# Optimization experiments

Measured on AMD Instinct MI355X. Metric: run time of the kernel, lower is better.

## Reference

```python
import jax, jax.numpy as jnp
import numpy as np

EPS = 1e-5  # nn.RMSNorm eps


def setup_inputs() -> dict:
    key = jax.random.key(0)
    ks = jax.random.split(key, 8)
    B, L, D, R = 4, 4096, 2048, 4
    return {
        "h": jax.random.normal(ks[0], (B, L, D), jnp.float32),
        "h_o": jax.random.normal(ks[1], (B, L, D), jnp.float32),
        "static_alpha": jax.random.normal(ks[2], (R, R + 1), jnp.float32),
        "static_beta": jax.random.normal(ks[3], (R,), jnp.float32),
        "dynamic_alpha_fn": jax.random.normal(ks[4], (D, R + 1), jnp.float32) * 0.02,
        "dynamic_alpha_scale": jax.random.uniform(ks[5], (1,), jnp.float32, 0.005, 0.02),
        "dynamic_beta_fn": jax.random.normal(ks[6], (D,), jnp.float32) * 0.02,
        "dynamic_beta_scale": jnp.array([0.01], jnp.float32),
        "rms_weight": jax.random.uniform(ks[7], (D,), jnp.float32, 0.5, 1.5),
    }


def reference(h, h_o, static_alpha, static_beta, dynamic_alpha_fn,
              dynamic_alpha_scale, dynamic_beta_fn, dynamic_beta_scale,
              rms_weight):
    # RMSNorm over last dim with learnable weight (dynamic branch only)
    h_norm = h * jax.lax.rsqrt(jnp.mean(h * h, axis=-1, keepdims=True) + EPS) * rms_weight

    # dynamic alpha: [B,L,rate+1] offset broadcast against static [rate,rate+1]
    alpha_offset = jnp.tanh(h_norm @ dynamic_alpha_fn) * dynamic_alpha_scale  # [B,L,R+1]
    alpha = alpha_offset[:, :, None, :] + static_alpha                        # [B,L,R,R+1]

    # dynamic beta: scalar offset per token broadcast against static [rate]
    beta_offset = jnp.tanh(h_norm @ dynamic_beta_fn) * dynamic_beta_scale     # [B,L] * [1]
    beta = beta_offset[..., None] + static_beta                               # [B,L,R]

    # connect_width: mix_h[b,l,c,d] = sum_r alpha[b,l,r,c] * h[b,l,d]
    mix_h = jnp.einsum('blrc,bld->blcd', alpha, h)                            # [B,L,R+1,D]

    # connect_depth: broadcast outer product beta x h_o plus old streams, sum over rate
    out = jnp.sum(beta[..., None] * h_o[:, :, None, :] + mix_h[:, :, 1:, :], axis=2)
    return out  # [B,L,D]
```

## Files before the change

### kernel.cpp

```cpp
#include <hip/hip_runtime.h>
#include <math.h>


constexpr int D    = 2048;
constexpr int RATE = 4;
constexpr float EPS = 1e-5f;
constexpr int TPB  = 8;
constexpr int NT   = 512;

__device__ __forceinline__ float fast_tanh(float x) {
    const float e = __expf(2.0f * x);
    return 1.0f - 2.0f / (e + 1.0f);
}

template<int CTRL>
__device__ __forceinline__ float dpp_add(float x) {
    int m = __builtin_amdgcn_update_dpp(0, __float_as_int(x), CTRL, 0xf, 0xf, true);
    return x + __int_as_float(m);
}

__device__ __forceinline__ float wave_sum_lane63(float x) {
    x = dpp_add<0x111>(x);
    x = dpp_add<0x112>(x);
    x = dpp_add<0x114>(x);
    x = dpp_add<0x118>(x);
    x = dpp_add<0x142>(x);
    x = dpp_add<0x143>(x);
    return x;
}

__device__ __forceinline__ void lds_barrier() {
    asm volatile("s_waitcnt lgkmcnt(0)" ::: "memory");
    __builtin_amdgcn_s_barrier();
    __builtin_amdgcn_sched_barrier(0);
}

__global__ __launch_bounds__(NT) void hyperconn_kernel(
    const float* __restrict__ h,
    const float* __restrict__ h_o,
    const float* __restrict__ sa,
    const float* __restrict__ sb,
    const float* __restrict__ fa,
    const float* __restrict__ a_sc,
    const float* __restrict__ fb,
    const float* __restrict__ b_sc,
    const float* __restrict__ w,
    float* __restrict__ out)
{
    const int tid  = threadIdx.x;
    const int d0   = tid * 4;
    const int wave = tid >> 6;
    const int lane = tid & 63;
    const size_t t0 = (size_t)blockIdx.x * TPB;

    const float4 wq  = *reinterpret_cast<const float4*>(w + d0);
    float tmp[20];
    #pragma unroll
    for (int q = 0; q < 5; ++q) {
        float4 t = *reinterpret_cast<const float4*>(fa + (size_t)d0 * 5 + q * 4);
        tmp[q*4+0]=t.x; tmp[q*4+1]=t.y; tmp[q*4+2]=t.z; tmp[q*4+3]=t.w;
    }
    const float4 fbq = *reinterpret_cast<const float4*>(fb + d0);

    float4 hA[TPB], oA[TPB];
    #pragma unroll
    for (int i = 0; i < TPB; ++i)
        hA[i] = *reinterpret_cast<const float4*>(h + (t0 + i) * D + d0);
    #pragma unroll
    for (int i = 0; i < TPB; ++i)
        oA[i] = *reinterpret_cast<const float4*>(h_o + (t0 + i) * D + d0);
    asm volatile("" ::: "memory");

    const float wv[4]  = {wq.x, wq.y, wq.z, wq.w};
    const float fbv[4] = {fbq.x, fbq.y, fbq.z, fbq.w};
    float fav[16];
    #pragma unroll
    for (int j = 0; j < 4; ++j)
        #pragma unroll
        for (int c = 0; c < 4; ++c)
            fav[j*4+c] = tmp[j*5 + 1 + c];

    const float a4 = a_sc[0] * (float)RATE;
    const float b4 = b_sc[0] * (float)RATE;
    float cs = 0.f;
    #pragma unroll
    for (int r = 0; r < RATE; ++r)
        #pragma unroll
        for (int c = 1; c <= RATE; ++c)
            cs += sa[r * (RATE + 1) + c];
    const float sbsum = sb[0] + sb[1] + sb[2] + sb[3];

    __shared__ float  red[TPB][48];
    __shared__ float2 s2[TPB];

    #pragma unroll
    for (int i = 0; i < TPB; ++i) {
        const float hv[4] = {hA[i].x, hA[i].y, hA[i].z, hA[i].w};
        float acc[6] = {0.f, 0.f, 0.f, 0.f, 0.f, 0.f};
        #pragma unroll
        for (int j = 0; j < 4; ++j) {
            const float x  = hv[j];
            const float xw = x * wv[j];
            acc[0] = fmaf(x,  x,          acc[0]);
            acc[1] = fmaf(xw, fav[j*4+0], acc[1]);
            acc[2] = fmaf(xw, fav[j*4+1], acc[2]);
            acc[3] = fmaf(xw, fav[j*4+2], acc[3]);
            acc[4] = fmaf(xw, fav[j*4+3], acc[4]);
            acc[5] = fmaf(xw, fbv[j],     acc[5]);
        }
        #pragma unroll
        for (int k = 0; k < 6; ++k) acc[k] = wave_sum_lane63(acc[k]);
        if (lane == 63) {
            #pragma unroll
            for (int k = 0; k < 6; ++k) red[i][wave * 6 + k] = acc[k];
        }
    }

    lds_barrier();

    {
        const int i = wave;
        float tot[6] = {0.f, 0.f, 0.f, 0.f, 0.f, 0.f};
        #pragma unroll
        for (int v = 0; v < 8; ++v)
            #pragma unroll
            for (int k = 0; k < 6; ++k)
                tot[k] += red[i][v * 6 + k];
        const float rms  = rsqrtf(tot[0] * (1.0f / (float)D) + EPS);
        const float s_h  = a4 * (fast_tanh(tot[1] * rms) + fast_tanh(tot[2] * rms) +
                                 fast_tanh(tot[3] * rms) + fast_tanh(tot[4] * rms)) + cs;
        const float s_ho = b4 * fast_tanh(tot[5] * rms) + sbsum;
        if (lane == 0) s2[i] = make_float2(s_h, s_ho);
    }

    lds_barrier();

    #pragma unroll
    for (int i = 0; i < TPB; ++i) {
        const float2 s = s2[i];
        const size_t base = (t0 + i) * D + d0;
        float4 r;
        r.x = fmaf(s.y, oA[i].x, s.x * hA[i].x);
        r.y = fmaf(s.y, oA[i].y, s.x * hA[i].y);
        r.z = fmaf(s.y, oA[i].z, s.x * hA[i].z);
        r.w = fmaf(s.y, oA[i].w, s.x * hA[i].w);
        *reinterpret_cast<float4*>(out + base) = r;
    }
}

extern "C" void kernel_launch(void* const* d_in, const int* in_sizes, int n_in,
                              void* d_out, int out_size, void* d_ws, size_t ws_size,
                              hipStream_t stream) {
    const float* h    = (const float*)d_in[0];
    const float* h_o  = (const float*)d_in[1];
    const float* sa   = (const float*)d_in[2];
    const float* sb   = (const float*)d_in[3];
    const float* fa   = (const float*)d_in[4];
    const float* a_sc = (const float*)d_in[5];
    const float* fb   = (const float*)d_in[6];
    const float* b_sc = (const float*)d_in[7];
    const float* w    = (const float*)d_in[8];
    float* out = (float*)d_out;

    const int ntok   = in_sizes[0] / D;
    const int blocks = ntok / TPB;
    hyperconn_kernel<<<blocks, NT, 0, stream>>>(h, h_o, sa, sb, fa, a_sc, fb, b_sc, w, out);
}
```

Measured before the change: 80.46 us.

## Assign whole tokens to waves with LDS weight tables, removing cross-wave reductions

Restructures the kernel so each wave processes four full tokens sequentially, with per-wave reductions finished via DPP and readlane broadcast instead of LDS plus two block barriers. Weight products (w*fa, w*fb) are precomputed once per block into a 40KB shared table read by every wave. This removes inter-wave synchronization and LDS reduction traffic, but adds LDS table setup per block, higher LDS usage that may limit occupancy, and serialized per-token loads within each wave.

```diff
diff --git a/kernel.cpp b/kernel.cpp
--- a/kernel.cpp
+++ b/kernel.cpp
@@ -5,8 +5,8 @@
 constexpr int D    = 2048;
 constexpr int RATE = 4;
 constexpr float EPS = 1e-5f;
-constexpr int TPB  = 8;
-constexpr int NT   = 512;
+constexpr int NT   = 256;
+constexpr int T    = 4;
 
 __device__ __forceinline__ float fast_tanh(float x) {
     const float e = __expf(2.0f * x);
@@ -29,6 +29,10 @@
     return x;
 }
 
+__device__ __forceinline__ float bcast63(float x) {
+    return __int_as_float(__builtin_amdgcn_readlane(__float_as_int(x), 63));
+}
+
 __device__ __forceinline__ void lds_barrier() {
     asm volatile("s_waitcnt lgkmcnt(0)" ::: "memory");
     __builtin_amdgcn_s_barrier();
@@ -48,37 +52,49 @@
     float* __restrict__ out)
 {
     const int tid  = threadIdx.x;
-    const int d0   = tid * 4;
     const int wave = tid >> 6;
     const int lane = tid & 63;
-    const size_t t0 = (size_t)blockIdx.x * TPB;
+    const int l4   = lane * 4;
 
-    const float4 wq  = *reinterpret_cast<const float4*>(w + d0);
-    float tmp[20];
+    const size_t tw = (size_t)blockIdx.x * (4 * T) + wave * T;
+
+    float4 hv[8];
     #pragma unroll
-    for (int q = 0; q < 5; ++q) {
-        float4 t = *reinterpret_cast<const float4*>(fa + (size_t)d0 * 5 + q * 4);
-        tmp[q*4+0]=t.x; tmp[q*4+1]=t.y; tmp[q*4+2]=t.z; tmp[q*4+3]=t.w;
+    for (int j = 0; j < 8; ++j)
+        hv[j] = *reinterpret_cast<const float4*>(h + tw * D + j * 256 + l4);
+
+    __shared__ float tabs[4 * D + D];
+
+    {
+        const int dd = tid * 8;
+        float fr[40];
+        #pragma unroll
+        for (int q = 0; q < 10; ++q) {
+            float4 t = *reinterpret_cast<const float4*>(fa + (size_t)dd * 5 + q * 4);
+            fr[q*4+0]=t.x; fr[q*4+1]=t.y; fr[q*4+2]=t.z; fr[q*4+3]=t.w;
+        }
+        const float4 w0 = *reinterpret_cast<const float4*>(w + dd);
+        const float4 w1 = *reinterpret_cast<const float4*>(w + dd + 4);
+        const float4 f0 = *reinterpret_cast<const float4*>(fb + dd);
+        const float4 f1 = *reinterpret_cast<const float4*>(fb + dd + 4);
+        const float ww[8] = {w0.x,w0.y,w0.z,w0.w,w1.x,w1.y,w1.z,w1.w};
+        const float ff[8] = {f0.x,f0.y,f0.z,f0.w,f1.x,f1.y,f1.z,f1.w};
+        #pragma unroll
+        for (int c = 0; c < 4; ++c) {
+            float4 v0, v1;
+            v0.x = ww[0]*fr[0*5+1+c]; v0.y = ww[1]*fr[1*5+1+c];
+            v0.z = ww[2]*fr[2*5+1+c]; v0.w = ww[3]*fr[3*5+1+c];
+            v1.x = ww[4]*fr[4*5+1+c]; v1.y = ww[5]*fr[5*5+1+c];
+            v1.z = ww[6]*fr[6*5+1+c]; v1.w = ww[7]*fr[7*5+1+c];
+            *reinterpret_cast<float4*>(&tabs[c * D + dd])     = v0;
+            *reinterpret_cast<float4*>(&tabs[c * D + dd + 4]) = v1;
+        }
+        float4 b0, b1;
+        b0.x = ww[0]*ff[0]; b0.y = ww[1]*ff[1]; b0.z = ww[2]*ff[2]; b0.w = ww[3]*ff[3];
+        b1.x = ww[4]*ff[4]; b1.y = ww[5]*ff[5]; b1.z = ww[6]*ff[6]; b1.w = ww[7]*ff[7];
+        *reinterpret_cast<float4*>(&tabs[4 * D + dd])     = b0;
+        *reinterpret_cast<float4*>(&tabs[4 * D + dd + 4]) = b1;
     }
-    const float4 fbq = *reinterpret_cast<const float4*>(fb + d0);
-
-    float4 hA[TPB], oA[TPB];
-    #pragma unroll
-    for (int i = 0; i < TPB; ++i)
-        hA[i] = *reinterpret_cast<const float4*>(h + (t0 + i) * D + d0);
-    #pragma unroll
-    for (int i = 0; i < TPB; ++i)
-        oA[i] = *reinterpret_cast<const float4*>(h_o + (t0 + i) * D + d0);
-    asm volatile("" ::: "memory");
-
-    const float wv[4]  = {wq.x, wq.y, wq.z, wq.w};
-    const float fbv[4] = {fbq.x, fbq.y, fbq.z, fbq.w};
-    float fav[16];
-    #pragma unroll
-    for (int j = 0; j < 4; ++j)
-        #pragma unroll
-        for (int c = 0; c < 4; ++c)
-            fav[j*4+c] = tmp[j*5 + 1 + c];
 
     const float a4 = a_sc[0] * (float)RATE;
     const float b4 = b_sc[0] * (float)RATE;
@@ -90,61 +106,65 @@
             cs += sa[r * (RATE + 1) + c];
     const float sbsum = sb[0] + sb[1] + sb[2] + sb[3];
 
-    __shared__ float  red[TPB][48];
-    __shared__ float2 s2[TPB];
-
-    #pragma unroll
-    for (int i = 0; i < TPB; ++i) {
-        const float hv[4] = {hA[i].x, hA[i].y, hA[i].z, hA[i].w};
-        float acc[6] = {0.f, 0.f, 0.f, 0.f, 0.f, 0.f};
-        #pragma unroll
-        for (int j = 0; j < 4; ++j) {
-            const float x  = hv[j];
-            const float xw = x * wv[j];
-            acc[0] = fmaf(x,  x,          acc[0]);
-            acc[1] = fmaf(xw, fav[j*4+0], acc[1]);
-            acc[2] = fmaf(xw, fav[j*4+1], acc[2]);
-            acc[3] = fmaf(xw, fav[j*4+2], acc[3]);
-            acc[4] = fmaf(xw, fav[j*4+3], acc[4]);
-            acc[5] = fmaf(xw, fbv[j],     acc[5]);
-        }
-        #pragma unroll
-        for (int k = 0; k < 6; ++k) acc[k] = wave_sum_lane63(acc[k]);
-        if (lane == 63) {
-            #pragma unroll
-            for (int k = 0; k < 6; ++k) red[i][wave * 6 + k] = acc[k];
-        }
-    }
-
-    lds_barrier();
-
-    {
-        const int i = wave;
-        float tot[6] = {0.f, 0.f, 0.f, 0.f, 0.f, 0.f};
-        #pragma unroll
-        for (int v = 0; v < 8; ++v)
-            #pragma unroll
-            for (int k = 0; k < 6; ++k)
-                tot[k] += red[i][v * 6 + k];
-        const float rms  = rsqrtf(tot[0] * (1.0f / (float)D) + EPS);
-        const float s_h  = a4 * (fast_tanh(tot[1] * rms) + fast_tanh(tot[2] * rms) +
-                                 fast_tanh(tot[3] * rms) + fast_tanh(tot[4] * rms)) + cs;
-        const float s_ho = b4 * fast_tanh(tot[5] * rms) + sbsum;
-        if (lane == 0) s2[i] = make_float2(s_h, s_ho);
-    }
-
     lds_barrier();
 
     #pragma unroll
-    for (int i = 0; i < TPB; ++i) {
-        const float2 s = s2[i];
-        const size_t base = (t0 + i) * D + d0;
-        float4 r;
-        r.x = fmaf(s.y, oA[i].x, s.x * hA[i].x);
-        r.y = fmaf(s.y, oA[i].y, s.x * hA[i].y);
-        r.z = fmaf(s.y, oA[i].z, s.x * hA[i].z);
-        r.w = fmaf(s.y, oA[i].w, s.x * hA[i].w);
-        *reinterpret_cast<float4*>(out + base) = r;
+    for (int i = 0; i < T; ++i) {
+        const size_t base = (tw + i) * D;
+
+        if (i > 0) {
+            #pragma unroll
+            for (int j = 0; j < 8; ++j)
+                hv[j] = *reinterpret_cast<const float4*>(h + base + j * 256 + l4);
+        }
+        float4 ov[8];
+        #pragma unroll
+        for (int j = 0; j < 8; ++j)
+            ov[j] = *reinterpret_cast<const float4*>(h_o + base + j * 256 + l4);
+
+        float acc[6] = {0.f, 0.f, 0.f, 0.f, 0.f, 0.f};
+        #pragma unroll
+        for (int j = 0; j < 8; ++j) {
+            const float4 hq = hv[j];
+            const int o = j * 256 + l4;
+            const float4 a0 = *reinterpret_cast<const float4*>(&tabs[0 * D + o]);
+            const float4 a1 = *reinterpret_cast<const float4*>(&tabs[1 * D + o]);
+            const float4 a2 = *reinterpret_cast<const float4*>(&tabs[2 * D + o]);
+            const float4 a3 = *reinterpret_cast<const float4*>(&tabs[3 * D + o]);
+            const float4 bq = *reinterpret_cast<const float4*>(&tabs[4 * D + o]);
+            acc[0] = fmaf(hq.x,hq.x,fmaf(hq.y,hq.y,fmaf(hq.z,hq.z,fmaf(hq.w,hq.w,acc[0]))));
+            acc[1] = fmaf(hq.x,a0.x,fmaf(hq.y,a0.y,fmaf(hq.z,a0.z,fmaf(hq.w,a0.w,acc[1]))));
+            acc[2] = fmaf(hq.x,a1.x,fmaf(hq.y,a1.y,fmaf(hq.z,a1.z,fmaf(hq.w,a1.w,acc[2]))));
+            acc[3] = fmaf(hq.x,a2.x,fmaf(hq.y,a2.y,fmaf(hq.z,a2.z,fmaf(hq.w,a2.w,acc[3]))));
+            acc[4] = fmaf(hq.x,a3.x,fmaf(hq.y,a3.y,fmaf(hq.z,a3.z,fmaf(hq.w,a3.w,acc[4]))));
+            acc[5] = fmaf(hq.x,bq.x,fmaf(hq.y,bq.y,fmaf(hq.z,bq.z,fmaf(hq.w,bq.w,acc[5]))));
+        }
+
+        #pragma unroll
+        for (int k = 0; k < 6; ++k) acc[k] = wave_sum_lane63(acc[k]);
+        const float tot0 = bcast63(acc[0]);
+        const float tot1 = bcast63(acc[1]);
+        const float tot2 = bcast63(acc[2]);
+        const float tot3 = bcast63(acc[3]);
+        const float tot4 = bcast63(acc[4]);
+        const float tot5 = bcast63(acc[5]);
+
+        const float rms  = rsqrtf(tot0 * (1.0f / (float)D) + EPS);
+        const float s_h  = a4 * (fast_tanh(tot1 * rms) + fast_tanh(tot2 * rms) +
+                                 fast_tanh(tot3 * rms) + fast_tanh(tot4 * rms)) + cs;
+        const float s_ho = b4 * fast_tanh(tot5 * rms) + sbsum;
+
+        #pragma unroll
+        for (int j = 0; j < 8; ++j) {
+            const float4 hq = hv[j];
+            const float4 oq = ov[j];
+            float4 r;
+            r.x = fmaf(s_ho, oq.x, s_h * hq.x);
+            r.y = fmaf(s_ho, oq.y, s_h * hq.y);
+            r.z = fmaf(s_ho, oq.z, s_h * hq.z);
+            r.w = fmaf(s_ho, oq.w, s_h * hq.w);
+            *reinterpret_cast<float4*>(out + base + j * 256 + l4) = r;
+        }
     }
 }
 
@@ -163,6 +183,6 @@
     float* out = (float*)d_out;
 
     const int ntok   = in_sizes[0] / D;
-    const int blocks = ntok / TPB;
+    const int blocks = ntok / (4 * T);
     hyperconn_kernel<<<blocks, NT, 0, stream>>>(h, h_o, sa, sb, fa, a_sc, fb, b_sc, w, out);
 }
```

Result: slower. 144.5 us (+79.6%).

## Halve tokens per block, defer h_o loads, prefold RMS weight into projections

Applied to the files above, without the earlier changes.

Tokens per block drop from 8 to 4 and launch bounds now request 8 blocks per CU, cutting register pressure and raising occupancy. The h_o tile is no longer preloaded into registers; it is loaded just before the output write, after the reductions. The RMSNorm weight is multiplied into the alpha and beta projection vectors once up front, which removes a multiply per element in the dot loop. Loading h_o late exposes its memory latency at the end of each block instead of overlapping it with the reduction, and each block now repeats the per-block parameter loads for fewer tokens.

```diff
diff --git a/kernel.cpp b/kernel.cpp
--- a/kernel.cpp
+++ b/kernel.cpp
@@ -5,7 +5,7 @@
 constexpr int D    = 2048;
 constexpr int RATE = 4;
 constexpr float EPS = 1e-5f;
-constexpr int TPB  = 8;
+constexpr int TPB  = 4;
 constexpr int NT   = 512;
 
 __device__ __forceinline__ float fast_tanh(float x) {
@@ -35,7 +35,7 @@
     __builtin_amdgcn_sched_barrier(0);
 }
 
-__global__ __launch_bounds__(NT) void hyperconn_kernel(
+__global__ __launch_bounds__(NT, 8) void hyperconn_kernel(
     const float* __restrict__ h,
     const float* __restrict__ h_o,
     const float* __restrict__ sa,
@@ -53,32 +53,30 @@
     const int lane = tid & 63;
     const size_t t0 = (size_t)blockIdx.x * TPB;
 
-    const float4 wq  = *reinterpret_cast<const float4*>(w + d0);
-    float tmp[20];
-    #pragma unroll
-    for (int q = 0; q < 5; ++q) {
-        float4 t = *reinterpret_cast<const float4*>(fa + (size_t)d0 * 5 + q * 4);
-        tmp[q*4+0]=t.x; tmp[q*4+1]=t.y; tmp[q*4+2]=t.z; tmp[q*4+3]=t.w;
-    }
-    const float4 fbq = *reinterpret_cast<const float4*>(fb + d0);
-
-    float4 hA[TPB], oA[TPB];
+    float4 hA[TPB];
     #pragma unroll
     for (int i = 0; i < TPB; ++i)
         hA[i] = *reinterpret_cast<const float4*>(h + (t0 + i) * D + d0);
-    #pragma unroll
-    for (int i = 0; i < TPB; ++i)
-        oA[i] = *reinterpret_cast<const float4*>(h_o + (t0 + i) * D + d0);
-    asm volatile("" ::: "memory");
 
-    const float wv[4]  = {wq.x, wq.y, wq.z, wq.w};
-    const float fbv[4] = {fbq.x, fbq.y, fbq.z, fbq.w};
-    float fav[16];
-    #pragma unroll
-    for (int j = 0; j < 4; ++j)
+    float fav[16], fbv[4];
+    {
+        const float4 wq = *reinterpret_cast<const float4*>(w + d0);
+        const float ww[4] = {wq.x, wq.y, wq.z, wq.w};
+        float tmp[20];
         #pragma unroll
-        for (int c = 0; c < 4; ++c)
-            fav[j*4+c] = tmp[j*5 + 1 + c];
+        for (int q = 0; q < 5; ++q) {
+            float4 t = *reinterpret_cast<const float4*>(fa + (size_t)d0 * 5 + q * 4);
+            tmp[q*4+0]=t.x; tmp[q*4+1]=t.y; tmp[q*4+2]=t.z; tmp[q*4+3]=t.w;
+        }
+        #pragma unroll
+        for (int j = 0; j < 4; ++j)
+            #pragma unroll
+            for (int c = 0; c < 4; ++c)
+                fav[j*4+c] = ww[j] * tmp[j*5 + 1 + c];
+        const float4 fq = *reinterpret_cast<const float4*>(fb + d0);
+        fbv[0] = ww[0]*fq.x; fbv[1] = ww[1]*fq.y;
+        fbv[2] = ww[2]*fq.z; fbv[3] = ww[3]*fq.w;
+    }
 
     const float a4 = a_sc[0] * (float)RATE;
     const float b4 = b_sc[0] * (float)RATE;
@@ -99,14 +97,13 @@
         float acc[6] = {0.f, 0.f, 0.f, 0.f, 0.f, 0.f};
         #pragma unroll
         for (int j = 0; j < 4; ++j) {
-            const float x  = hv[j];
-            const float xw = x * wv[j];
-            acc[0] = fmaf(x,  x,          acc[0]);
-            acc[1] = fmaf(xw, fav[j*4+0], acc[1]);
-            acc[2] = fmaf(xw, fav[j*4+1], acc[2]);
-            acc[3] = fmaf(xw, fav[j*4+2], acc[3]);
-            acc[4] = fmaf(xw, fav[j*4+3], acc[4]);
-            acc[5] = fmaf(xw, fbv[j],     acc[5]);
+            const float x = hv[j];
+            acc[0] = fmaf(x, x,          acc[0]);
+            acc[1] = fmaf(x, fav[j*4+0], acc[1]);
+            acc[2] = fmaf(x, fav[j*4+1], acc[2]);
+            acc[3] = fmaf(x, fav[j*4+2], acc[3]);
+            acc[4] = fmaf(x, fav[j*4+3], acc[4]);
+            acc[5] = fmaf(x, fbv[j],     acc[5]);
         }
         #pragma unroll
         for (int k = 0; k < 6; ++k) acc[k] = wave_sum_lane63(acc[k]);
@@ -118,7 +115,7 @@
 
     lds_barrier();
 
-    {
+    if (wave < TPB) {
         const int i = wave;
         float tot[6] = {0.f, 0.f, 0.f, 0.f, 0.f, 0.f};
         #pragma unroll
@@ -139,11 +136,12 @@
     for (int i = 0; i < TPB; ++i) {
         const float2 s = s2[i];
         const size_t base = (t0 + i) * D + d0;
+        const float4 oq = *reinterpret_cast<const float4*>(h_o + base);
         float4 r;
-        r.x = fmaf(s.y, oA[i].x, s.x * hA[i].x);
-        r.y = fmaf(s.y, oA[i].y, s.x * hA[i].y);
-        r.z = fmaf(s.y, oA[i].z, s.x * hA[i].z);
-        r.w = fmaf(s.y, oA[i].w, s.x * hA[i].w);
+        r.x = fmaf(s.y, oq.x, s.x * hA[i].x);
+        r.y = fmaf(s.y, oq.y, s.x * hA[i].y);
+        r.z = fmaf(s.y, oq.z, s.x * hA[i].z);
+        r.w = fmaf(s.y, oq.w, s.x * hA[i].w);
         *reinterpret_cast<float4*>(out + base) = r;
     }
 }
```

Result: faster. 77.24 us, median of 2 (-4.0%).
